# Kernel tuning notes

Measured on AMD Instinct MI355X. Metric: run time of the kernel, lower is better.

Reference implementation:

```python
import jax, jax.numpy as jnp
import numpy as np

EPS = 1.1920929e-07  # torch RMSNorm default eps = finfo(float32).eps

D = 2048
N_LAYERS = 12
RANK = 16
VOCAB = 32000
B, T = 2, 2048


def _rmsnorm(x, w):
    # x * rsqrt(mean(x^2) + eps) * w
    ms = jnp.mean(jnp.square(x), axis=-1, keepdims=True)
    return x * jax.lax.rsqrt(ms + EPS) * w


def setup_inputs() -> dict:
    key = jax.random.key(0)
    ks = jax.random.split(key, 9)
    n_funcs = N_LAYERS * 2
    inp = {
        "tokens": jax.random.randint(ks[0], (B, T), 0, VOCAB, dtype=jnp.int32),
        "hologram_real": 0.01 * jax.random.normal(ks[1], (D, D), jnp.float32),
        "hologram_imag": 0.01 * jax.random.normal(ks[2], (D, D), jnp.float32),
        "key_a_real": 0.02 * jax.random.normal(ks[3], (n_funcs, RANK, D), jnp.float32),
        "key_a_imag": 0.02 * jax.random.normal(ks[4], (n_funcs, RANK, D), jnp.float32),
        "key_b_real": 0.02 * jax.random.normal(ks[5], (n_funcs, RANK, D), jnp.float32),
        "key_b_imag": 0.02 * jax.random.normal(ks[6], (n_funcs, RANK, D), jnp.float32),
        "layer_scale": 0.1 * jnp.ones((n_funcs,), jnp.float32),
        "norm_w": jnp.ones((N_LAYERS, 2, D), jnp.float32),
        "embed": jax.random.normal(ks[7], (VOCAB, D), jnp.float32),
        "lm_head_w": (1.0 / np.sqrt(D)) * jax.random.normal(ks[8], (VOCAB, D), jnp.float32),
        "final_norm_w": jnp.ones((D,), jnp.float32),
    }
    return inp


def _reconstruct_all(hr, hi, kar, kai, kbr, kbi, scale):
    # pattern = sum_r ka[r] outer conj(kb[r]); complex math in real arithmetic:
    #   Re(pattern)[d,e] = sum_r kar*kbr + kai*kbi
    #   Im(pattern)[d,e] = sum_r kai*kbr - kar*kbi
    pr = jnp.einsum('frd,fre->fde', kar, kbr) + jnp.einsum('frd,fre->fde', kai, kbi)
    pi = jnp.einsum('frd,fre->fde', kai, kbr) - jnp.einsum('frd,fre->fde', kar, kbi)
    # W = Re(hologram * pattern) * scale = (hr*pr - hi*pi) * scale
    return (hr[None] * pr - hi[None] * pi) * scale[:, None, None]  # [n_funcs, D, D]


def reference(tokens, hologram_real, hologram_imag, key_a_real, key_a_imag,
              key_b_real, key_b_imag, layer_scale, norm_w, embed, lm_head_w,
              final_norm_w):
    x = embed[tokens].astype(jnp.float32)  # [B, T, D]
    W = _reconstruct_all(hologram_real, hologram_imag, key_a_real, key_a_imag,
                         key_b_real, key_b_imag, layer_scale)
    W_attn = W[0::2]  # [n_layers, D, D]
    W_ffn = W[1::2]

    def layer(x, per):
        Wa, Wf, nw = per
        h = _rmsnorm(x, nw[0])
        x = x + jnp.einsum('btd,ed->bte', h, Wa)  # F.linear: h @ Wa.T
        h = _rmsnorm(x, nw[1])
        x = x + jax.nn.silu(jnp.einsum('btd,ed->bte', h, Wf))
        return x, None

    x, _ = jax.lax.scan(layer, x, (W_attn, W_ffn, norm_w))
    x = _rmsnorm(x, final_norm_w)
    return jnp.einsum('btd,vd->btv', x, lm_head_w)  # logits [B, T, V]
```

## Files before the change

kernel.cpp:

```cpp
#include <hip/hip_runtime.h>
#include <hip/hip_bf16.h>

#define DD 2048
#define NF 24
#define NROWS 4096
#define VOCAB_N 32000
#define EPS_F 1.1920929e-07f

typedef __attribute__((ext_vector_type(8))) __bf16 bf16x8;
typedef __attribute__((ext_vector_type(4))) float f32x4;

__device__ __forceinline__ unsigned short f2bf(float f) {
  union { float f; unsigned int u; } v; v.f = f;
  unsigned int r = v.u + 0x7fffu + ((v.u >> 16) & 1u);
  return (unsigned short)(r >> 16);
}
__device__ __forceinline__ float bf2f(unsigned short u) {
  union { unsigned int i; float f; } v; v.i = ((unsigned int)u) << 16; return v.f;
}

__device__ __forceinline__ void gload_lds16(const void* g, void* l) {
  __builtin_amdgcn_global_load_lds(
      (const __attribute__((address_space(1))) void*)g,
      (__attribute__((address_space(3))) void*)l, 16, 0, 0);
}

__global__ __launch_bounds__(256) void k_gather(const int* __restrict__ tok,
                                                const float* __restrict__ embed,
                                                unsigned short* __restrict__ h0,
                                                float* __restrict__ p0) {
  const int row = blockIdx.x, tid = threadIdx.x;
  const int t = tok[row];
  const float4* s = (const float4*)(embed + (size_t)t * DD);
  const float4 a = s[tid], b = s[tid + 256];
  float ss = a.x * a.x + a.y * a.y + a.z * a.z + a.w * a.w +
             b.x * b.x + b.y * b.y + b.z * b.z + b.w * b.w;
#pragma unroll
  for (int m = 32; m; m >>= 1) ss += __shfl_xor(ss, m);
  __shared__ float part[4];
  if ((tid & 63) == 0) part[tid >> 6] = ss;
  __syncthreads();
  if (tid == 0) p0[(size_t)row * 8] = part[0] + part[1] + part[2] + part[3];
  ushort4 o0, o1;
  o0.x = f2bf(a.x); o0.y = f2bf(a.y); o0.z = f2bf(a.z); o0.w = f2bf(a.w);
  o1.x = f2bf(b.x); o1.y = f2bf(b.y); o1.z = f2bf(b.z); o1.w = f2bf(b.w);
  ushort4* d = (ushort4*)(h0 + (size_t)row * DD);
  d[tid] = o0;
  d[tid + 256] = o1;
}

__global__ __launch_bounds__(256) void k_wrec(
    const float* __restrict__ hr, const float* __restrict__ hi,
    const float* __restrict__ kar, const float* __restrict__ kai,
    const float* __restrict__ kbr, const float* __restrict__ kbi,
    const float* __restrict__ scale, const float* __restrict__ nw,
    unsigned short* __restrict__ W) {
  __shared__ float KAR[16][132], KAI[16][132];
  __shared__ float KBR[16][68], KBI[16][68];
  __shared__ unsigned short Wt[128][72];
  const int tid = threadIdx.x;
  const int lane = tid & 63, w = tid >> 6;
  const int fr = lane & 15, g = lane >> 4;
  const int o0 = blockIdx.x * 128, i0 = blockIdx.y * 64;

  float hrg[2][4][4], hig[2][4][4];
#pragma unroll
  for (int of = 0; of < 2; ++of)
#pragma unroll
    for (int jj = 0; jj < 4; ++jj) {
      const size_t orow = (size_t)(o0 + w * 32 + of * 16 + g * 4 + jj) * DD + i0;
#pragma unroll
      for (int fi = 0; fi < 4; ++fi) {
        hrg[of][jj][fi] = hr[orow + fi * 16 + fr];
        hig[of][jj][fi] = hi[orow + fi * 16 + fr];
      }
    }

  const int sr = tid >> 4;
  const int sca = (tid & 15) * 8;
  const int scb = (tid & 15) * 4;
  const int rlo = (g & 1) * 8;

  for (int f = 0; f < NF; ++f) {
    __syncthreads();
    {
      const size_t ga = ((size_t)f * 16 + sr) * DD;
      *(float4*)&KAR[sr][sca]     = *(const float4*)&kar[ga + o0 + sca];
      *(float4*)&KAR[sr][sca + 4] = *(const float4*)&kar[ga + o0 + sca + 4];
      *(float4*)&KAI[sr][sca]     = *(const float4*)&kai[ga + o0 + sca];
      *(float4*)&KAI[sr][sca + 4] = *(const float4*)&kai[ga + o0 + sca + 4];
      *(float4*)&KBR[sr][scb]     = *(const float4*)&kbr[ga + i0 + scb];
      *(float4*)&KBI[sr][scb]     = *(const float4*)&kbi[ga + i0 + scb];
    }
    __syncthreads();
    bf16x8 aPr[2], aPi[2], bF[4];
#pragma unroll
    for (int of = 0; of < 2; ++of) {
      const int oc = w * 32 + of * 16 + fr;
      union { bf16x8 v; unsigned short u[8]; } pu, pv;
#pragma unroll
      for (int j = 0; j < 8; ++j) {
        const float ka = KAR[rlo + j][oc];
        const float kb = KAI[rlo + j][oc];
        pu.u[j] = f2bf((g < 2) ? ka : kb);
        pv.u[j] = f2bf((g < 2) ? kb : -ka);
      }
      aPr[of] = pu.v; aPi[of] = pv.v;
    }
#pragma unroll
    for (int fi = 0; fi < 4; ++fi) {
      const int ic = fi * 16 + fr;
      union { bf16x8 v; unsigned short u[8]; } pb;
#pragma unroll
      for (int j = 0; j < 8; ++j) {
        const float vr = KBR[rlo + j][ic];
        const float vi = KBI[rlo + j][ic];
        pb.u[j] = f2bf((g < 2) ? vr : vi);
      }
      bF[fi] = pb.v;
    }
    const float sc = scale[f];
    float nwv[4];
#pragma unroll
    for (int fi = 0; fi < 4; ++fi) nwv[fi] = nw[(size_t)f * DD + i0 + fi * 16 + fr];
#pragma unroll
    for (int of = 0; of < 2; ++of)
#pragma unroll
      for (int fi = 0; fi < 4; ++fi) {
        const f32x4 z = (f32x4){0.f, 0.f, 0.f, 0.f};
        const f32x4 cr = __builtin_amdgcn_mfma_f32_16x16x32_bf16(aPr[of], bF[fi], z, 0, 0, 0);
        const f32x4 ci = __builtin_amdgcn_mfma_f32_16x16x32_bf16(aPi[of], bF[fi], z, 0, 0, 0);
#pragma unroll
        for (int jj = 0; jj < 4; ++jj) {
          const float wv = (hrg[of][jj][fi] * cr[jj] - hig[of][jj][fi] * ci[jj]) * sc * nwv[fi];
          Wt[w * 32 + of * 16 + g * 4 + jj][fi * 16 + fr] = f2bf(wv);
        }
      }
    __syncthreads();
    {
      const int r = tid >> 1, hh = tid & 1;
      unsigned short* dst = W + ((size_t)f * DD + o0 + r) * DD + i0 + hh * 32;
#pragma unroll
      for (int qq = 0; qq < 4; ++qq)
        *(uint4*)(dst + qq * 8) = *(const uint4*)&Wt[r][hh * 32 + qq * 8];
    }
  }
}

template <int ACT>
__global__ __launch_bounds__(512, 2) void k_gemmL(const unsigned short* __restrict__ Hin,
                                                  const unsigned short* __restrict__ B,
                                                  unsigned short* __restrict__ Hout,
                                                  const float* __restrict__ Pin,
                                                  float* __restrict__ Pout) {
  constexpr int NTILE = DD / 64;
  __shared__ unsigned short lsA[3][8192];
  __shared__ unsigned short lsB[3][16384];
  __shared__ float invS[128];
  __shared__ float rsum[128];
  const int tid = threadIdx.x;
  const int lane = tid & 63, wave = tid >> 6;
  const int wm = wave >> 2, wn = wave & 3;
  const int bid = blockIdx.x;
  const int swz = (bid & 7) * 32 + (bid >> 3);
  const int t0 = (swz >> 3) * 128;
  const int n0 = (swz & 7) * 256;
  const unsigned short* Ab = Hin + (size_t)t0 * DD;
  const unsigned short* Bb = B + (size_t)n0 * DD;
  const int fr = lane & 15, g = lane >> 4;
  const int srow8 = tid >> 3, sslot = tid & 7;

#define LSTG_A(slot, tile)                                                          \
  { _Pragma("unroll")                                                               \
    for (int l = 0; l < 2; ++l) {                                                   \
      const int rt = l * 64 + srow8;                                                \
      gload_lds16(Ab + (size_t)rt * DD + (tile) * 64 + ((sslot ^ (rt & 7)) << 3),   \
                  &lsA[slot][rt * 64 + sslot * 8]);                                 \
    } }
#define LSTG_B(slot, h, tile)                                                       \
  { _Pragma("unroll")                                                               \
    for (int l = 0; l < 2; ++l) {                                                   \
      const int rt = (h) * 128 + l * 64 + srow8;                                    \
      gload_lds16(Bb + (size_t)rt * DD + (tile) * 64 + ((sslot ^ (rt & 7)) << 3),   \
                  &lsB[slot][rt * 64 + sslot * 8]);                                 \
    } }
#define LRD_A(slot, mi, ks)                                                         \
  (*(const bf16x8*)&lsA[slot][(wm * 64 + (mi) * 16 + fr) * 64 +                     \
                              ((((ks) * 4 + g) ^ ((wm * 64 + (mi) * 16 + fr) & 7)) << 3)])
#define LRD_B(slot, ni, ks)                                                         \
  (*(const bf16x8*)&lsB[slot][(wn * 64 + (ni) * 16 + fr) * 64 +                     \
                              ((((ks) * 4 + g) ^ ((wn * 64 + (ni) * 16 + fr) & 7)) << 3)])

  f32x4 acc[4][4];
#pragma unroll
  for (int i = 0; i < 4; ++i)
#pragma unroll
    for (int j = 0; j < 4; ++j) acc[i][j] = (f32x4){0.f, 0.f, 0.f, 0.f};

  bf16x8 aF[4][2], bF[4][2];

#define LTILE(t, sc, sp)                                                            \
  {                                                                                 \
    const bool st = (t) + 2 < NTILE;                                                \
    _Pragma("unroll")                                                               \
    for (int mi = 0; mi < 4; ++mi) { _Pragma("unroll")                              \
      for (int ks = 0; ks < 2; ++ks) aF[mi][ks] = LRD_A(sc, mi, ks); }              \
    _Pragma("unroll")                                                               \
    for (int ni = 0; ni < 4; ++ni) { _Pragma("unroll")                              \
      for (int ks = 0; ks < 2; ++ks) bF[ni][ks] = LRD_B(sc, ni, ks); }              \
    if (st) { LSTG_A(sp, (t) + 2); LSTG_B(sp, 0, (t) + 2); LSTG_B(sp, 1, (t) + 2); }\
    if (st) asm volatile("s_waitcnt vmcnt(6)" ::: "memory");                        \
    else    asm volatile("s_waitcnt vmcnt(0)" ::: "memory");                        \
    __builtin_amdgcn_s_barrier();                                                   \
    asm volatile("s_waitcnt lgkmcnt(0)" ::: "memory");                              \
    __builtin_amdgcn_s_setprio(1);                                                  \
    _Pragma("unroll")                                                               \
    for (int ks = 0; ks < 2; ++ks) { _Pragma("unroll")                              \
      for (int mi = 0; mi < 4; ++mi) { _Pragma("unroll")                            \
        for (int ni = 0; ni < 4; ++ni)                                              \
          acc[mi][ni] = __builtin_amdgcn_mfma_f32_16x16x32_bf16(                    \
              aF[mi][ks], bF[ni][ks], acc[mi][ni], 0, 0, 0); } }                    \
    __builtin_amdgcn_s_setprio(0);                                                  \
    __builtin_amdgcn_s_barrier();                                                   \
  }

  LSTG_A(0, 0); LSTG_B(0, 0, 0); LSTG_B(0, 1, 0);
  LSTG_A(1, 1); LSTG_B(1, 0, 1); LSTG_B(1, 1, 1);
  if (tid < 128) {
    const float* pr = Pin + (size_t)(t0 + tid) * 8;
    const float s = pr[0] + pr[1] + pr[2] + pr[3] + pr[4] + pr[5] + pr[6] + pr[7];
    invS[tid] = rsqrtf(s * (1.f / DD) + EPS_F);
  }
  asm volatile("s_waitcnt vmcnt(6)" ::: "memory");
  __builtin_amdgcn_s_barrier();

  for (int tb = 0; tb < 30; tb += 3) {
    LTILE(tb, 0, 2);
    LTILE(tb + 1, 1, 0);
    LTILE(tb + 2, 2, 1);
  }
  LTILE(30, 0, 2);
  LTILE(31, 1, 0);
#undef LTILE
#undef LRD_A
#undef LRD_B
#undef LSTG_A
#undef LSTG_B

  __syncthreads();
  if (tid < 128) rsum[tid] = 0.f;
  __syncthreads();
  const int panel = n0 >> 8;
#pragma unroll
  for (int mi = 0; mi < 4; ++mi) {
#pragma unroll
    for (int j = 0; j < 4; ++j) {
      const int lr = wm * 64 + mi * 16 + g * 4 + j;
      const float iv = invS[lr];
      float racc = 0.f;
#pragma unroll
      for (int ni = 0; ni < 4; ++ni) {
        const size_t idx = (size_t)(t0 + lr) * DD + (n0 + wn * 64 + ni * 16 + fr);
        const float v = acc[mi][ni][j] * iv;
        const float old = bf2f(Hin[idx]);
        float nv;
        if (ACT == 0) nv = old + v;
        else          nv = old + v / (1.f + __expf(-v));
        Hout[idx] = f2bf(nv);
        racc += nv * nv;
      }
      racc += __shfl_xor(racc, 1);
      racc += __shfl_xor(racc, 2);
      racc += __shfl_xor(racc, 4);
      racc += __shfl_xor(racc, 8);
      if (fr == 0) atomicAdd(&rsum[lr], racc);
    }
  }
  __syncthreads();
  if (tid < 128) Pout[(size_t)(t0 + tid) * 8 + panel] = rsum[tid];
}

template <int BM>
__global__ __launch_bounds__(512, 2) void k_gemm8(const unsigned short* __restrict__ A,
                                                  const unsigned short* __restrict__ B,
                                                  float* __restrict__ C, const int ldc,
                                                  const int npan,
                                                  const float* __restrict__ Pin) {
  constexpr int HALF = BM / 2;
  constexpr int MI = BM / 32;
  constexpr int MQ = MI / 2;
  constexpr int A_LOADS = HALF / 64;
  constexpr int NTILE = DD / 64;
  constexpr int NITER = NTILE / 2;

  __shared__ unsigned short lsA[2][BM * 64];
  __shared__ unsigned short lsB[2][256 * 64];
  __shared__ float invS[BM];

  const int tid = threadIdx.x;
  const int lane = tid & 63, wave = tid >> 6;
  const int wm = wave >> 2, wn = wave & 3;
  const int bid = blockIdx.x;
  const int swz = (bid & 7) * (gridDim.x >> 3) + (bid >> 3);
  const int t0 = (swz / npan) * BM;
  const int n0 = (swz % npan) * 256;
  const unsigned short* Ab = A + (size_t)t0 * DD;
  const unsigned short* Bb = B + (size_t)n0 * DD;
  const int fr = lane & 15, g = lane >> 4;
  const int srow8 = tid >> 3, sslot = tid & 7;

#define STG_A(buf, h, tile)                                                         \
  { _Pragma("unroll")                                                               \
    for (int l = 0; l < A_LOADS; ++l) {                                             \
      const int rt = (h) * HALF + l * 64 + srow8;                                   \
      gload_lds16(Ab + (size_t)rt * DD + (tile) * 64 + ((sslot ^ (rt & 7)) << 3),   \
                  &lsA[buf][rt * 64 + sslot * 8]);                                  \
    } }
#define STG_B(buf, h, tile)                                                         \
  { _Pragma("unroll")                                                               \
    for (int l = 0; l < 2; ++l) {                                                   \
      const int rt = (h) * 128 + l * 64 + srow8;                                    \
      gload_lds16(Bb + (size_t)rt * DD + (tile) * 64 + ((sslot ^ (rt & 7)) << 3),   \
                  &lsB[buf][rt * 64 + sslot * 8]);                                  \
    } }
#define VM_G3()                                                                     \
  { if constexpr (BM == 256) asm volatile("s_waitcnt vmcnt(6)" ::: "memory");       \
    else                     asm volatile("s_waitcnt vmcnt(5)" ::: "memory"); }
#define VM_G7()                                                                     \
  { if constexpr (BM == 256) asm volatile("s_waitcnt vmcnt(8)" ::: "memory");       \
    else                     asm volatile("s_waitcnt vmcnt(6)" ::: "memory"); }
#define VM_PRO()                                                                    \
  { if constexpr (BM == 256) asm volatile("s_waitcnt vmcnt(8)" ::: "memory");       \
    else                     asm volatile("s_waitcnt vmcnt(6)" ::: "memory"); }
#define VM_ZERO() asm volatile("s_waitcnt vmcnt(0)" ::: "memory")

  f32x4 acc[MI][4];
#pragma unroll
  for (int i = 0; i < MI; ++i)
#pragma unroll
    for (int j = 0; j < 4; ++j) acc[i][j] = (f32x4){0.f, 0.f, 0.f, 0.f};

  bf16x8 aF[MQ][2];
  bf16x8 bF[2][2][2];

#define RD_A(buf, mi, ks)                                                           \
  (*(const bf16x8*)&lsA[buf][(wm * HALF + (mi) * 16 + fr) * 64 +                    \
                             ((((ks) * 4 + g) ^ ((wm * HALF + (mi) * 16 + fr) & 7)) << 3)])
#define RD_B(buf, ni, ks)                                                           \
  (*(const bf16x8*)&lsB[buf][(wn * 64 + (ni) * 16 + fr) * 64 +                      \
                             ((((ks) * 4 + g) ^ ((wn * 64 + (ni) * 16 + fr) & 7)) << 3)])

#define PHASE(buf, mh, nh, LA, LB, STAGES, VMK)                                     \
  {                                                                                 \
    if (LA) { _Pragma("unroll")                                                     \
      for (int q = 0; q < MQ; ++q) { _Pragma("unroll")                              \
        for (int ks = 0; ks < 2; ++ks) aF[q][ks] = RD_A(buf, (mh) * MQ + q, ks); } }\
    if (LB) { _Pragma("unroll")                                                     \
      for (int q = 0; q < 2; ++q) { _Pragma("unroll")                               \
        for (int ks = 0; ks < 2; ++ks) bF[nh][q][ks] = RD_B(buf, (nh) * 2 + q, ks); } } \
    STAGES;                                                                         \
    VMK;                                                                            \
    __builtin_amdgcn_s_barrier();                                                   \
    asm volatile("s_waitcnt lgkmcnt(0)" ::: "memory");                              \
    __builtin_amdgcn_s_setprio(1);                                                  \
    _Pragma("unroll")                                                               \
    for (int ks = 0; ks < 2; ++ks) { _Pragma("unroll")                              \
      for (int q = 0; q < MQ; ++q) { _Pragma("unroll")                              \
        for (int nq = 0; nq < 2; ++nq)                                              \
          acc[(mh) * MQ + q][(nh) * 2 + nq] = __builtin_amdgcn_mfma_f32_16x16x32_bf16( \
              aF[q][ks], bF[nh][nq][ks], acc[(mh) * MQ + q][(nh) * 2 + nq], 0, 0, 0); } } \
    __builtin_amdgcn_s_setprio(0);                                                  \
    __builtin_amdgcn_s_barrier();                                                   \
  }

  STG_B(0, 0, 0); STG_B(0, 1, 0); STG_A(0, 0, 0); STG_A(0, 1, 0);
  STG_B(1, 0, 1); STG_B(1, 1, 1); STG_A(1, 0, 1); STG_A(1, 1, 1);
  if (tid < BM) {
    const float* pr = Pin + (size_t)(t0 + tid) * 8;
    const float s = pr[0] + pr[1] + pr[2] + pr[3] + pr[4] + pr[5] + pr[6] + pr[7];
    invS[tid] = rsqrtf(s * (1.f / DD) + EPS_F);
  }
  VM_PRO();
  __builtin_amdgcn_s_barrier();

  for (int i = 0; i < NITER; ++i) {
    const int T2 = 2 * i + 2, T3 = 2 * i + 3;
    const bool s2 = T2 < NTILE, s3 = T3 < NTILE;
    PHASE(0, 0, 0, true,  true,  {}, {});
    PHASE(0, 0, 1, false, true,  {}, {});
    PHASE(0, 1, 1, true,  false, { if (s2) { STG_B(0, 0, T2); STG_B(0, 1, T2); } }, {});
    PHASE(0, 1, 0, false, false, { if (s2) STG_A(0, 0, T2); },
          { if (s2) VM_G3() else VM_ZERO(); });
    PHASE(1, 0, 0, true,  true,  { if (s2) STG_A(0, 1, T2); }, {});
    PHASE(1, 0, 1, false, true,  {}, {});
    PHASE(1, 1, 1, true,  false, { if (s3) { STG_B(1, 0, T3); STG_B(1, 1, T3); } }, {});
    PHASE(1, 1, 0, false, false, { if (s3) { STG_A(1, 0, T3); STG_A(1, 1, T3); } },
          { if (s3) VM_G7() else VM_ZERO(); });
  }
#undef PHASE
#undef RD_A
#undef RD_B
#undef STG_A
#undef STG_B
#undef VM_G3
#undef VM_G7
#undef VM_PRO
#undef VM_ZERO

#pragma unroll
  for (int mi = 0; mi < MI; ++mi) {
#pragma unroll
    for (int ni = 0; ni < 4; ++ni) {
      const int ocol = n0 + wn * 64 + ni * 16 + fr;
#pragma unroll
      for (int j = 0; j < 4; ++j) {
        const int lr = wm * HALF + mi * 16 + g * 4 + j;
        const size_t idx = (size_t)(t0 + lr) * ldc + ocol;
        C[idx] = invS[lr] * acc[mi][ni][j];
      }
    }
  }
}

__global__ void k_cvt(const float* __restrict__ in, const float* __restrict__ fnw,
                      unsigned short* __restrict__ out, int n4) {
  int i = blockIdx.x * blockDim.x + threadIdx.x;
  const int stride = gridDim.x * blockDim.x;
  for (; i < n4; i += stride) {
    const float4 v = ((const float4*)in)[i];
    const float4 w = ((const float4*)fnw)[i & 511];
    ushort4 o;
    o.x = f2bf(v.x * w.x); o.y = f2bf(v.y * w.y);
    o.z = f2bf(v.z * w.z); o.w = f2bf(v.w * w.w);
    ((ushort4*)out)[i] = o;
  }
}

extern "C" void kernel_launch(void* const* d_in, const int* in_sizes, int n_in,
                              void* d_out, int out_size, void* d_ws, size_t ws_size,
                              hipStream_t stream) {
  (void)in_sizes; (void)n_in; (void)out_size; (void)ws_size;
  const int* tokens = (const int*)d_in[0];
  const float* hr = (const float*)d_in[1];
  const float* hi = (const float*)d_in[2];
  const float* kar = (const float*)d_in[3];
  const float* kai = (const float*)d_in[4];
  const float* kbr = (const float*)d_in[5];
  const float* kbi = (const float*)d_in[6];
  const float* lscale = (const float*)d_in[7];
  const float* norm_w = (const float*)d_in[8];
  const float* embed = (const float*)d_in[9];
  const float* lm = (const float*)d_in[10];
  const float* fnw = (const float*)d_in[11];
  float* out = (float*)d_out;
  char* ws = (char*)d_ws;

  unsigned short* W = (unsigned short*)ws;
  float* P0 = (float*)(ws + 201326592);
  float* P1 = P0 + (size_t)NROWS * 8;
  unsigned short* hA = (unsigned short*)(ws + 201326592 + 262144);
  unsigned short* hB = (unsigned short*)d_out;
  unsigned short* lmb = W;

  hipMemsetAsync(P0, 0, (size_t)NROWS * 8 * sizeof(float), stream);
  k_gather<<<NROWS, 256, 0, stream>>>(tokens, embed, hA, P0);
  k_wrec<<<dim3(16, 32), 256, 0, stream>>>(hr, hi, kar, kai, kbr, kbi, lscale,
                                           norm_w, W);
  const unsigned short* cin = hA;
  unsigned short* cout = hB;
  const float* pin = P0;
  float* pout = P1;
  for (int l = 0; l < 12; ++l) {
    k_gemmL<0><<<256, 512, 0, stream>>>(cin, W + (size_t)(2 * l) * DD * DD, cout, pin, pout);
    { const unsigned short* tc = cin; cin = cout; cout = (unsigned short*)tc;
      const float* tp = pin; pin = pout; pout = (float*)tp; }
    k_gemmL<1><<<256, 512, 0, stream>>>(cin, W + (size_t)(2 * l + 1) * DD * DD, cout, pin, pout);
    { const unsigned short* tc = cin; cin = cout; cout = (unsigned short*)tc;
      const float* tp = pin; pin = pout; pout = (float*)tp; }
  }
  k_cvt<<<2048, 256, 0, stream>>>(lm, fnw, lmb, VOCAB_N * DD / 4);
  k_gemm8<256><<<2000, 512, 0, stream>>>(cin, lmb, out, VOCAB_N, 125, pin);
}
```

Baseline: 1.835 ms.

## Fuse 24 per-layer GEMM launches into one persistent cooperative kernel

Replaces the 24 separate k_gemmL launches with a single cooperative kernel that loops over all layers and uses a grid-wide sync between them, swapping activation and partial-sum buffers in-kernel. This targets kernel launch overhead and the tail/ramp gaps between dependent launches. In exchange, grid.sync costs a global barrier per layer, the activation type becomes a runtime branch, and the whole grid of 256 blocks must be co-resident. After an even number of swaps the final output stays in hA/P0, which the LM head now reads directly.

```diff
diff --git a/kernel.cpp b/kernel.cpp
--- a/kernel.cpp
+++ b/kernel.cpp
@@ -1,5 +1,8 @@
 #include <hip/hip_runtime.h>
 #include <hip/hip_bf16.h>
+#include <hip/hip_cooperative_groups.h>
+
+namespace cg = cooperative_groups;
 
 #define DD 2048
 #define NF 24
@@ -147,17 +150,16 @@
   }
 }
 
-template <int ACT>
-__global__ __launch_bounds__(512, 2) void k_gemmL(const unsigned short* __restrict__ Hin,
-                                                  const unsigned short* __restrict__ B,
-                                                  unsigned short* __restrict__ Hout,
-                                                  const float* __restrict__ Pin,
-                                                  float* __restrict__ Pout) {
+__global__ __launch_bounds__(512, 2) void k_layers(
+    const unsigned short* __restrict__ Wall,
+    unsigned short* __restrict__ hA_, unsigned short* __restrict__ hB_,
+    float* __restrict__ P0_, float* __restrict__ P1_) {
   constexpr int NTILE = DD / 64;
   __shared__ unsigned short lsA[3][8192];
   __shared__ unsigned short lsB[3][16384];
   __shared__ float invS[128];
   __shared__ float rsum[128];
+  cg::grid_group gg = cg::this_grid();
   const int tid = threadIdx.x;
   const int lane = tid & 63, wave = tid >> 6;
   const int wm = wave >> 2, wn = wave & 3;
@@ -165,10 +167,14 @@
   const int swz = (bid & 7) * 32 + (bid >> 3);
   const int t0 = (swz >> 3) * 128;
   const int n0 = (swz & 7) * 256;
-  const unsigned short* Ab = Hin + (size_t)t0 * DD;
-  const unsigned short* Bb = B + (size_t)n0 * DD;
   const int fr = lane & 15, g = lane >> 4;
   const int srow8 = tid >> 3, sslot = tid & 7;
+  const int panel = n0 >> 8;
+
+  const unsigned short* Hin = hA_;
+  unsigned short* Hout = hB_;
+  const float* Pin = P0_;
+  float* Pout = P1_;
 
 #define LSTG_A(slot, tile)                                                          \
   { _Pragma("unroll")                                                               \
@@ -190,15 +196,6 @@
 #define LRD_B(slot, ni, ks)                                                         \
   (*(const bf16x8*)&lsB[slot][(wn * 64 + (ni) * 16 + fr) * 64 +                     \
                               ((((ks) * 4 + g) ^ ((wn * 64 + (ni) * 16 + fr) & 7)) << 3)])
-
-  f32x4 acc[4][4];
-#pragma unroll
-  for (int i = 0; i < 4; ++i)
-#pragma unroll
-    for (int j = 0; j < 4; ++j) acc[i][j] = (f32x4){0.f, 0.f, 0.f, 0.f};
-
-  bf16x8 aF[4][2], bF[4][2];
-
 #define LTILE(t, sc, sp)                                                            \
   {                                                                                 \
     const bool st = (t) + 2 < NTILE;                                                \
@@ -224,60 +221,75 @@
     __builtin_amdgcn_s_barrier();                                                   \
   }
 
-  LSTG_A(0, 0); LSTG_B(0, 0, 0); LSTG_B(0, 1, 0);
-  LSTG_A(1, 1); LSTG_B(1, 0, 1); LSTG_B(1, 1, 1);
-  if (tid < 128) {
-    const float* pr = Pin + (size_t)(t0 + tid) * 8;
-    const float s = pr[0] + pr[1] + pr[2] + pr[3] + pr[4] + pr[5] + pr[6] + pr[7];
-    invS[tid] = rsqrtf(s * (1.f / DD) + EPS_F);
-  }
-  asm volatile("s_waitcnt vmcnt(6)" ::: "memory");
-  __builtin_amdgcn_s_barrier();
-
-  for (int tb = 0; tb < 30; tb += 3) {
-    LTILE(tb, 0, 2);
-    LTILE(tb + 1, 1, 0);
-    LTILE(tb + 2, 2, 1);
-  }
-  LTILE(30, 0, 2);
-  LTILE(31, 1, 0);
+  for (int lyr = 0; lyr < NF; ++lyr) {
+    const unsigned short* Ab = Hin + (size_t)t0 * DD;
+    const unsigned short* Bb = Wall + (size_t)lyr * DD * DD + (size_t)n0 * DD;
+
+    f32x4 acc[4][4];
+#pragma unroll
+    for (int i = 0; i < 4; ++i)
+#pragma unroll
+      for (int j = 0; j < 4; ++j) acc[i][j] = (f32x4){0.f, 0.f, 0.f, 0.f};
+    bf16x8 aF[4][2], bF[4][2];
+
+    LSTG_A(0, 0); LSTG_B(0, 0, 0); LSTG_B(0, 1, 0);
+    LSTG_A(1, 1); LSTG_B(1, 0, 1); LSTG_B(1, 1, 1);
+    if (tid < 128) {
+      const float* pr = Pin + (size_t)(t0 + tid) * 8;
+      const float s = pr[0] + pr[1] + pr[2] + pr[3] + pr[4] + pr[5] + pr[6] + pr[7];
+      invS[tid] = rsqrtf(s * (1.f / DD) + EPS_F);
+    }
+    asm volatile("s_waitcnt vmcnt(6)" ::: "memory");
+    __builtin_amdgcn_s_barrier();
+
+    for (int tb = 0; tb < 30; tb += 3) {
+      LTILE(tb, 0, 2);
+      LTILE(tb + 1, 1, 0);
+      LTILE(tb + 2, 2, 1);
+    }
+    LTILE(30, 0, 2);
+    LTILE(31, 1, 0);
+
+    __syncthreads();
+    if (tid < 128) rsum[tid] = 0.f;
+    __syncthreads();
+    const bool silu = (lyr & 1) != 0;
+#pragma unroll
+    for (int mi = 0; mi < 4; ++mi) {
+#pragma unroll
+      for (int j = 0; j < 4; ++j) {
+        const int lr = wm * 64 + mi * 16 + g * 4 + j;
+        const float iv = invS[lr];
+        float racc = 0.f;
+#pragma unroll
+        for (int ni = 0; ni < 4; ++ni) {
+          const size_t idx = (size_t)(t0 + lr) * DD + (n0 + wn * 64 + ni * 16 + fr);
+          const float v = acc[mi][ni][j] * iv;
+          const float old = bf2f(Hin[idx]);
+          const float nv = silu ? (old + v / (1.f + __expf(-v))) : (old + v);
+          Hout[idx] = f2bf(nv);
+          racc += nv * nv;
+        }
+        racc += __shfl_xor(racc, 1);
+        racc += __shfl_xor(racc, 2);
+        racc += __shfl_xor(racc, 4);
+        racc += __shfl_xor(racc, 8);
+        if (fr == 0) atomicAdd(&rsum[lr], racc);
+      }
+    }
+    __syncthreads();
+    if (tid < 128) Pout[(size_t)(t0 + tid) * 8 + panel] = rsum[tid];
+
+    if (lyr != NF - 1) gg.sync();
+
+    const unsigned short* th = Hin; Hin = Hout; Hout = (unsigned short*)th;
+    const float* tp = Pin; Pin = Pout; Pout = (float*)tp;
+  }
 #undef LTILE
 #undef LRD_A
 #undef LRD_B
 #undef LSTG_A
 #undef LSTG_B
-
-  __syncthreads();
-  if (tid < 128) rsum[tid] = 0.f;
-  __syncthreads();
-  const int panel = n0 >> 8;
-#pragma unroll
-  for (int mi = 0; mi < 4; ++mi) {
-#pragma unroll
-    for (int j = 0; j < 4; ++j) {
-      const int lr = wm * 64 + mi * 16 + g * 4 + j;
-      const float iv = invS[lr];
-      float racc = 0.f;
-#pragma unroll
-      for (int ni = 0; ni < 4; ++ni) {
-        const size_t idx = (size_t)(t0 + lr) * DD + (n0 + wn * 64 + ni * 16 + fr);
-        const float v = acc[mi][ni][j] * iv;
-        const float old = bf2f(Hin[idx]);
-        float nv;
-        if (ACT == 0) nv = old + v;
-        else          nv = old + v / (1.f + __expf(-v));
-        Hout[idx] = f2bf(nv);
-        racc += nv * nv;
-      }
-      racc += __shfl_xor(racc, 1);
-      racc += __shfl_xor(racc, 2);
-      racc += __shfl_xor(racc, 4);
-      racc += __shfl_xor(racc, 8);
-      if (fr == 0) atomicAdd(&rsum[lr], racc);
-    }
-  }
-  __syncthreads();
-  if (tid < 128) Pout[(size_t)(t0 + tid) * 8 + panel] = rsum[tid];
 }
 
 template <int BM>
@@ -466,18 +478,11 @@
   k_gather<<<NROWS, 256, 0, stream>>>(tokens, embed, hA, P0);
   k_wrec<<<dim3(16, 32), 256, 0, stream>>>(hr, hi, kar, kai, kbr, kbi, lscale,
                                            norm_w, W);
-  const unsigned short* cin = hA;
-  unsigned short* cout = hB;
-  const float* pin = P0;
-  float* pout = P1;
-  for (int l = 0; l < 12; ++l) {
-    k_gemmL<0><<<256, 512, 0, stream>>>(cin, W + (size_t)(2 * l) * DD * DD, cout, pin, pout);
-    { const unsigned short* tc = cin; cin = cout; cout = (unsigned short*)tc;
-      const float* tp = pin; pin = pout; pout = (float*)tp; }
-    k_gemmL<1><<<256, 512, 0, stream>>>(cin, W + (size_t)(2 * l + 1) * DD * DD, cout, pin, pout);
-    { const unsigned short* tc = cin; cin = cout; cout = (unsigned short*)tc;
-      const float* tp = pin; pin = pout; pout = (float*)tp; }
+  {
+    const unsigned short* Wc = W;
+    void* args[] = {(void*)&Wc, (void*)&hA, (void*)&hB, (void*)&P0, (void*)&P1};
+    hipLaunchCooperativeKernel((void*)k_layers, dim3(256), dim3(512), args, 0, stream);
   }
   k_cvt<<<2048, 256, 0, stream>>>(lm, fnw, lmb, VOCAB_N * DD / 4);
-  k_gemm8<256><<<2000, 512, 0, stream>>>(cin, lmb, out, VOCAB_N, 125, pin);
-}
+  k_gemm8<256><<<2000, 512, 0, stream>>>(hA, lmb, out, VOCAB_N, 125, P0);
+}
```

Measured after the change: 2.666 ms. 1.45x slower.
